# Kernel tuning notes

Measured on AMD Instinct MI355X. Metric: run time of the kernel, lower is better.

The kernel has to match this reference:

```python
import jax, jax.numpy as jnp
import numpy as np

N = 100000  # number of nodes
E = 3200000  # number of edges (avg degree 32)


def spmm(rows, cols, vals, Y):
    # sparse A (COO) @ dense Y : gather rows of Y at cols, scale, scatter-add to rows
    return jax.ops.segment_sum(vals[:, None] * Y[cols], rows, num_segments=N)


def setup_inputs() -> dict:
    key = jax.random.key(0)
    kx, kr, kc, kv, k0, k1 = jax.random.split(key, 6)
    X = jax.random.normal(kx, (N, 512), dtype=jnp.float32)
    edge_rows = jax.random.randint(kr, (E,), 0, N, dtype=jnp.int32)
    edge_cols = jax.random.randint(kc, (E,), 0, N, dtype=jnp.int32)
    edge_vals = jax.random.uniform(kv, (E,), dtype=jnp.float32)
    W0 = jax.random.normal(k0, (512, 256), dtype=jnp.float32) * 0.05
    W1 = jax.random.normal(k1, (256, 64), dtype=jnp.float32) * 0.05
    return {"X": X, "edge_rows": edge_rows, "edge_cols": edge_cols,
            "edge_vals": edge_vals, "W0": W0, "W1": W1}


def reference(X, edge_rows, edge_cols, edge_vals, W0, W1):
    # layer 1: A_hat @ (X W0), relu
    H1 = jax.nn.relu(spmm(edge_rows, edge_cols, edge_vals, X @ W0))  # [N, H]
    # layer 2: A_hat @ (H1 W1), softmax over classes
    Z = spmm(edge_rows, edge_cols, edge_vals, H1 @ W1)  # [N, F]
    return jax.nn.softmax(Z, axis=-1)
```

## Files before the change

### kernel.cpp

```cpp
#include <hip/hip_runtime.h>
#include <hip/hip_bf16.h>
#include <hip/hip_fp16.h>
#include <cstdint>

#define N_NODES 100000
#define N_EDGES 3200000
#define F_IN    512
#define F_HID   256
#define F_OUT   64
#define CAP     96

typedef _Float16 half8_t __attribute__((ext_vector_type(8)));
typedef _Float16 half4_t __attribute__((ext_vector_type(4)));
typedef float    float4_t __attribute__((ext_vector_type(4)));


__global__ __launch_bounds__(256) void zero_cursors_kernel(int* __restrict__ cursor, int n) {
    int i = blockIdx.x * 256 + threadIdx.x;
    if (i < n) cursor[i] = 0;
}

__global__ __launch_bounds__(256) void ell_scatter_kernel(
    const int* __restrict__ rows, const int* __restrict__ cols,
    const float* __restrict__ vals, int* __restrict__ cursor,
    int* __restrict__ ell_col, float* __restrict__ ell_val, int e_count) {
    int e = blockIdx.x * 256 + threadIdx.x;
    if (e >= e_count) return;
    int r = rows[e];
    int p = atomicAdd(&cursor[r], 1);
    if (p < CAP) {
        ell_col[(size_t)r * CAP + p] = cols[e];
        ell_val[(size_t)r * CAP + p] = vals[e];
    }
}


__global__ __launch_bounds__(256) void convert_w_kernel(
    const float* __restrict__ W0, const float* __restrict__ W1,
    _Float16* __restrict__ W0T, _Float16* __restrict__ W1T) {
    int i = blockIdx.x * 256 + threadIdx.x;
    if (i < F_HID * F_IN) {
        int n = i >> 9, k = i & 511;
        W0T[i] = (_Float16)W0[k * F_HID + n];
    }
    int j = i - F_HID * F_IN;
    if (j >= 0 && j < F_OUT * F_HID) {
        int n = j >> 8, k = j & 255;
        W1T[j] = (_Float16)W1[k * F_OUT + n];
    }
}


__global__ __launch_bounds__(256) void gemm1_mfma_kernel(
    const float* __restrict__ X, const _Float16* __restrict__ W0T,
    _Float16* __restrict__ H0) {
    const int wave = threadIdx.x >> 6;
    const int lane = threadIdx.x & 63;
    const int l15  = lane & 15;
    const int quad = lane >> 4;
    const int m0   = blockIdx.x * 64;
    const int n0   = wave * 64;

    float4_t acc[4][4] = {};

    int row[4];
    #pragma unroll
    for (int mt = 0; mt < 4; mt++) {
        int r = m0 + mt * 16 + l15;
        row[mt] = r < N_NODES ? r : N_NODES - 1;
    }

    for (int k0 = 0; k0 < F_IN; k0 += 32) {
        const int kk = k0 + quad * 8;
        half8_t b[4];
        #pragma unroll
        for (int nt = 0; nt < 4; nt++)
            b[nt] = *(const half8_t*)(W0T + (size_t)(n0 + nt * 16 + l15) * F_IN + kk);

        half8_t a[4];
        #pragma unroll
        for (int mt = 0; mt < 4; mt++) {
            const float* p = X + (size_t)row[mt] * F_IN + kk;
            float4_t lo = *(const float4_t*)p;
            float4_t hi = *(const float4_t*)(p + 4);
            half8_t f;
            f[0] = (_Float16)lo[0]; f[1] = (_Float16)lo[1];
            f[2] = (_Float16)lo[2]; f[3] = (_Float16)lo[3];
            f[4] = (_Float16)hi[0]; f[5] = (_Float16)hi[1];
            f[6] = (_Float16)hi[2]; f[7] = (_Float16)hi[3];
            a[mt] = f;
        }

        #pragma unroll
        for (int mt = 0; mt < 4; mt++)
            #pragma unroll
            for (int nt = 0; nt < 4; nt++)
                acc[mt][nt] = __builtin_amdgcn_mfma_f32_16x16x32_f16(
                    a[mt], b[nt], acc[mt][nt], 0, 0, 0);
    }

    #pragma unroll
    for (int mt = 0; mt < 4; mt++)
        #pragma unroll
        for (int reg = 0; reg < 4; reg++) {
            int m = m0 + mt * 16 + quad * 4 + reg;
            if (m < N_NODES) {
                #pragma unroll
                for (int nt = 0; nt < 4; nt++)
                    H0[(size_t)m * F_HID + n0 + nt * 16 + l15] =
                        (_Float16)acc[mt][nt][reg];
            }
        }
}


__global__ __launch_bounds__(256) void gemm2_mfma_kernel(
    const _Float16* __restrict__ H1, const _Float16* __restrict__ W1T,
    _Float16* __restrict__ H2) {
    const int wave = threadIdx.x >> 6;
    const int lane = threadIdx.x & 63;
    const int l15  = lane & 15;
    const int quad = lane >> 4;
    const int m0   = blockIdx.x * 64 + wave * 16;

    int r = m0 + l15;
    if (r >= N_NODES) r = N_NODES - 1;

    float4_t acc[4] = {};

    for (int k0 = 0; k0 < F_HID; k0 += 32) {
        const int kk = k0 + quad * 8;
        half8_t a = *(const half8_t*)(H1 + (size_t)r * F_HID + kk);
        #pragma unroll
        for (int nt = 0; nt < 4; nt++) {
            half8_t b = *(const half8_t*)(W1T + (size_t)(nt * 16 + l15) * F_HID + kk);
            acc[nt] = __builtin_amdgcn_mfma_f32_16x16x32_f16(a, b, acc[nt], 0, 0, 0);
        }
    }

    #pragma unroll
    for (int reg = 0; reg < 4; reg++) {
        int m = m0 + quad * 4 + reg;
        if (m < N_NODES) {
            #pragma unroll
            for (int nt = 0; nt < 4; nt++)
                H2[(size_t)m * F_OUT + nt * 16 + l15] = (_Float16)acc[nt][reg];
        }
    }
}


__global__ __launch_bounds__(256) void spmm_relu_kernel(
    const _Float16* __restrict__ H0, const int* __restrict__ ell_col,
    const float* __restrict__ ell_val, const int* __restrict__ cursor,
    _Float16* __restrict__ H1) {
    const int r = blockIdx.x * 4 + (threadIdx.x >> 6);
    const int t = threadIdx.x & 63;
    int n = cursor[r]; if (n > CAP) n = CAP;
    const int*   cols = ell_col + (size_t)r * CAP;
    const float* vals = ell_val + (size_t)r * CAP;
    const half4_t* H0v = (const half4_t*)H0;

    float4_t acc = {};
    int j = 0;
    for (; j + 4 <= n; j += 4) {
        int4   c = *(const int4*)(cols + j);
        float4 v = *(const float4*)(vals + j);
        half4_t g0 = H0v[(size_t)c.x * 64 + t];
        half4_t g1 = H0v[(size_t)c.y * 64 + t];
        half4_t g2 = H0v[(size_t)c.z * 64 + t];
        half4_t g3 = H0v[(size_t)c.w * 64 + t];
        #pragma unroll
        for (int i = 0; i < 4; i++) {
            acc[i] = fmaf(v.x, (float)g0[i], acc[i]);
            acc[i] = fmaf(v.y, (float)g1[i], acc[i]);
            acc[i] = fmaf(v.z, (float)g2[i], acc[i]);
            acc[i] = fmaf(v.w, (float)g3[i], acc[i]);
        }
    }
    for (; j < n; j++) {
        half4_t g = H0v[(size_t)cols[j] * 64 + t];
        float vv = vals[j];
        #pragma unroll
        for (int i = 0; i < 4; i++) acc[i] = fmaf(vv, (float)g[i], acc[i]);
    }
    half4_t o;
    #pragma unroll
    for (int i = 0; i < 4; i++) o[i] = (_Float16)fmaxf(acc[i], 0.f);
    ((half4_t*)H1)[(size_t)r * 64 + t] = o;
}


__global__ __launch_bounds__(256) void spmm_softmax_kernel(
    const _Float16* __restrict__ H2, const int* __restrict__ ell_col,
    const float* __restrict__ ell_val, const int* __restrict__ cursor,
    float* __restrict__ out) {
    const int lane = threadIdx.x & 63;
    const int r = blockIdx.x * 4 + (threadIdx.x >> 6);
    int n = cursor[r]; if (n > CAP) n = CAP;
    const int*   cols = ell_col + (size_t)r * CAP;
    const float* vals = ell_val + (size_t)r * CAP;
    float acc = 0.f;
    int j = 0;
    for (; j + 4 <= n; j += 4) {
        int4   c = *(const int4*)(cols + j);
        float4 v = *(const float4*)(vals + j);
        acc = fmaf(v.x, (float)H2[(size_t)c.x * F_OUT + lane], acc);
        acc = fmaf(v.y, (float)H2[(size_t)c.y * F_OUT + lane], acc);
        acc = fmaf(v.z, (float)H2[(size_t)c.z * F_OUT + lane], acc);
        acc = fmaf(v.w, (float)H2[(size_t)c.w * F_OUT + lane], acc);
    }
    for (; j < n; j++)
        acc = fmaf(vals[j], (float)H2[(size_t)cols[j] * F_OUT + lane], acc);

    float m = acc;
    #pragma unroll
    for (int o = 32; o >= 1; o >>= 1) m = fmaxf(m, __shfl_xor(m, o, 64));
    float e = expf(acc - m);
    float s = e;
    #pragma unroll
    for (int o = 32; o >= 1; o >>= 1) s += __shfl_xor(s, o, 64);
    out[(size_t)r * F_OUT + lane] = e / s;
}


extern "C" void kernel_launch(void* const* d_in, const int* in_sizes, int n_in,
                              void* d_out, int out_size, void* d_ws, size_t ws_size,
                              hipStream_t stream) {
    const float* X     = (const float*)d_in[0];
    const int*   erows = (const int*)  d_in[1];
    const int*   ecols = (const int*)  d_in[2];
    const float* evals = (const float*)d_in[3];
    const float* W0    = (const float*)d_in[4];
    const float* W1    = (const float*)d_in[5];
    float* out = (float*)d_out;

    char* p = (char*)d_ws;
    _Float16* H0  = (_Float16*)p; p += (size_t)N_NODES * F_HID * 2;
    _Float16* H1  = (_Float16*)p; p += (size_t)N_NODES * F_HID * 2;
    _Float16* H2  = (_Float16*)p; p += (size_t)N_NODES * F_OUT * 2;
    _Float16* W0T = (_Float16*)p; p += (size_t)F_HID * F_IN * 2;
    _Float16* W1T = (_Float16*)p; p += (size_t)F_OUT * F_HID * 2;
    int*   cursor  = (int*)p;     p += (size_t)N_NODES * 4;
    int*   ell_col = (int*)p;     p += (size_t)N_NODES * CAP * 4;
    float* ell_val = (float*)p;

    zero_cursors_kernel<<<(N_NODES + 255) / 256, 256, 0, stream>>>(cursor, N_NODES);
    ell_scatter_kernel<<<(N_EDGES + 255) / 256, 256, 0, stream>>>(
        erows, ecols, evals, cursor, ell_col, ell_val, N_EDGES);
    convert_w_kernel<<<(F_HID * F_IN + F_OUT * F_HID + 255) / 256, 256, 0, stream>>>(
        W0, W1, W0T, W1T);

    gemm1_mfma_kernel<<<(N_NODES + 63) / 64, 256, 0, stream>>>(X, W0T, H0);

    spmm_relu_kernel<<<N_NODES / 4, 256, 0, stream>>>(H0, ell_col, ell_val, cursor, H1);

    gemm2_mfma_kernel<<<(N_NODES + 63) / 64, 256, 0, stream>>>(H1, W1T, H2);

    spmm_softmax_kernel<<<N_NODES / 4, 256, 0, stream>>>(H2, ell_col, ell_val, cursor, out);
}
```

Baseline: 989.0 us.

## Fuse scatter with GEMM1, SpMM1 with GEMM2, and interleave ELL col/val

```diff
diff --git a/kernel.cpp b/kernel.cpp
--- a/kernel.cpp
+++ b/kernel.cpp
@@ -10,35 +10,21 @@
 #define F_OUT   64
 #define CAP     96
 
+#define G_SCATTER 12500
+#define G_GEMM1   3125
+#define LDS_STRIDE 272
+
 typedef _Float16 half8_t __attribute__((ext_vector_type(8)));
 typedef _Float16 half4_t __attribute__((ext_vector_type(4)));
 typedef float    float4_t __attribute__((ext_vector_type(4)));
 
 
-__global__ __launch_bounds__(256) void zero_cursors_kernel(int* __restrict__ cursor, int n) {
+__global__ __launch_bounds__(256) void prep_kernel(
+    const float* __restrict__ W0, const float* __restrict__ W1,
+    _Float16* __restrict__ W0T, _Float16* __restrict__ W1T,
+    int* __restrict__ cursor) {
     int i = blockIdx.x * 256 + threadIdx.x;
-    if (i < n) cursor[i] = 0;
-}
-
-__global__ __launch_bounds__(256) void ell_scatter_kernel(
-    const int* __restrict__ rows, const int* __restrict__ cols,
-    const float* __restrict__ vals, int* __restrict__ cursor,
-    int* __restrict__ ell_col, float* __restrict__ ell_val, int e_count) {
-    int e = blockIdx.x * 256 + threadIdx.x;
-    if (e >= e_count) return;
-    int r = rows[e];
-    int p = atomicAdd(&cursor[r], 1);
-    if (p < CAP) {
-        ell_col[(size_t)r * CAP + p] = cols[e];
-        ell_val[(size_t)r * CAP + p] = vals[e];
-    }
-}
-
-
-__global__ __launch_bounds__(256) void convert_w_kernel(
-    const float* __restrict__ W0, const float* __restrict__ W1,
-    _Float16* __restrict__ W0T, _Float16* __restrict__ W1T) {
-    int i = blockIdx.x * 256 + threadIdx.x;
+    if (i < N_NODES) cursor[i] = 0;
     if (i < F_HID * F_IN) {
         int n = i >> 9, k = i & 511;
         W0T[i] = (_Float16)W0[k * F_HID + n];
@@ -51,24 +37,31 @@
 }
 
 
-__global__ __launch_bounds__(256) void gemm1_mfma_kernel(
+__global__ __launch_bounds__(256, 6) void mega_kernel(
+    const int* __restrict__ erows, const int* __restrict__ ecols,
+    const float* __restrict__ evals, int* __restrict__ cursor,
+    int2* __restrict__ ell,
     const float* __restrict__ X, const _Float16* __restrict__ W0T,
     _Float16* __restrict__ H0) {
+
+    if (blockIdx.x < G_SCATTER) {
+        int e = blockIdx.x * 256 + threadIdx.x;
+        int r = erows[e];
+        int p = atomicAdd(&cursor[r], 1);
+        if (p < CAP)
+            ell[(size_t)r * CAP + p] = make_int2(ecols[e], __float_as_int(evals[e]));
+        return;
+    }
+
+    const int blk  = blockIdx.x - G_SCATTER;
     const int wave = threadIdx.x >> 6;
     const int lane = threadIdx.x & 63;
     const int l15  = lane & 15;
     const int quad = lane >> 4;
-    const int m0   = blockIdx.x * 64;
+    const int m0   = blk * 32;
     const int n0   = wave * 64;
 
-    float4_t acc[4][4] = {};
-
-    int row[4];
-    #pragma unroll
-    for (int mt = 0; mt < 4; mt++) {
-        int r = m0 + mt * 16 + l15;
-        row[mt] = r < N_NODES ? r : N_NODES - 1;
-    }
+    float4_t acc[2][4] = {};
 
     for (int k0 = 0; k0 < F_IN; k0 += 32) {
         const int kk = k0 + quad * 8;
@@ -77,10 +70,10 @@
         for (int nt = 0; nt < 4; nt++)
             b[nt] = *(const half8_t*)(W0T + (size_t)(n0 + nt * 16 + l15) * F_IN + kk);
 
-        half8_t a[4];
-        #pragma unroll
-        for (int mt = 0; mt < 4; mt++) {
-            const float* p = X + (size_t)row[mt] * F_IN + kk;
+        half8_t a[2];
+        #pragma unroll
+        for (int mt = 0; mt < 2; mt++) {
+            const float* p = X + (size_t)(m0 + mt * 16 + l15) * F_IN + kk;
             float4_t lo = *(const float4_t*)p;
             float4_t hi = *(const float4_t*)(p + 4);
             half8_t f;
@@ -92,7 +85,7 @@
         }
 
         #pragma unroll
-        for (int mt = 0; mt < 4; mt++)
+        for (int mt = 0; mt < 2; mt++)
             #pragma unroll
             for (int nt = 0; nt < 4; nt++)
                 acc[mt][nt] = __builtin_amdgcn_mfma_f32_16x16x32_f16(
@@ -100,118 +93,108 @@
     }
 
     #pragma unroll
-    for (int mt = 0; mt < 4; mt++)
+    for (int mt = 0; mt < 2; mt++)
         #pragma unroll
         for (int reg = 0; reg < 4; reg++) {
             int m = m0 + mt * 16 + quad * 4 + reg;
-            if (m < N_NODES) {
-                #pragma unroll
-                for (int nt = 0; nt < 4; nt++)
-                    H0[(size_t)m * F_HID + n0 + nt * 16 + l15] =
-                        (_Float16)acc[mt][nt][reg];
+            #pragma unroll
+            for (int nt = 0; nt < 4; nt++)
+                H0[(size_t)m * F_HID + n0 + nt * 16 + l15] =
+                    (_Float16)acc[mt][nt][reg];
+        }
+}
+
+
+__global__ __launch_bounds__(256) void spmm_relu_gemm2_kernel(
+    const _Float16* __restrict__ H0, const int2* __restrict__ ell,
+    const int* __restrict__ cursor, const _Float16* __restrict__ W1T,
+    _Float16* __restrict__ H2) {
+    __shared__ _Float16 hrow[16][LDS_STRIDE];
+
+    const int wave = threadIdx.x >> 6;
+    const int t    = threadIdx.x & 63;
+    const int base = blockIdx.x * 16;
+    const half4_t* H0v = (const half4_t*)H0;
+
+    for (int rr = 0; rr < 4; rr++) {
+        const int local = wave * 4 + rr;
+        const int r = base + local;
+        int n = cursor[r]; if (n > CAP) n = CAP;
+        const int2* cv = ell + (size_t)r * CAP;
+
+        float4_t acc = {};
+        int j = 0;
+        for (; j + 4 <= n; j += 4) {
+            int4 e0 = *(const int4*)(cv + j);
+            int4 e1 = *(const int4*)(cv + j + 2);
+            half4_t g0 = H0v[(size_t)e0.x * 64 + t];
+            half4_t g1 = H0v[(size_t)e0.z * 64 + t];
+            half4_t g2 = H0v[(size_t)e1.x * 64 + t];
+            half4_t g3 = H0v[(size_t)e1.z * 64 + t];
+            float v0 = __int_as_float(e0.y), v1 = __int_as_float(e0.w);
+            float v2 = __int_as_float(e1.y), v3 = __int_as_float(e1.w);
+            #pragma unroll
+            for (int i = 0; i < 4; i++) {
+                acc[i] = fmaf(v0, (float)g0[i], acc[i]);
+                acc[i] = fmaf(v1, (float)g1[i], acc[i]);
+                acc[i] = fmaf(v2, (float)g2[i], acc[i]);
+                acc[i] = fmaf(v3, (float)g3[i], acc[i]);
             }
         }
-}
-
-
-__global__ __launch_bounds__(256) void gemm2_mfma_kernel(
-    const _Float16* __restrict__ H1, const _Float16* __restrict__ W1T,
-    _Float16* __restrict__ H2) {
-    const int wave = threadIdx.x >> 6;
-    const int lane = threadIdx.x & 63;
-    const int l15  = lane & 15;
-    const int quad = lane >> 4;
-    const int m0   = blockIdx.x * 64 + wave * 16;
-
-    int r = m0 + l15;
-    if (r >= N_NODES) r = N_NODES - 1;
-
-    float4_t acc[4] = {};
-
+        for (; j < n; j++) {
+            int2 e = cv[j];
+            half4_t g = H0v[(size_t)e.x * 64 + t];
+            float vv = __int_as_float(e.y);
+            #pragma unroll
+            for (int i = 0; i < 4; i++) acc[i] = fmaf(vv, (float)g[i], acc[i]);
+        }
+        half4_t o;
+        #pragma unroll
+        for (int i = 0; i < 4; i++) o[i] = (_Float16)fmaxf(acc[i], 0.f);
+        *(half4_t*)(&hrow[local][t * 4]) = o;
+    }
+    __syncthreads();
+
+    const int l15  = t & 15;
+    const int quad = t >> 4;
+    float4_t acc2 = {};
+    #pragma unroll
     for (int k0 = 0; k0 < F_HID; k0 += 32) {
         const int kk = k0 + quad * 8;
-        half8_t a = *(const half8_t*)(H1 + (size_t)r * F_HID + kk);
-        #pragma unroll
-        for (int nt = 0; nt < 4; nt++) {
-            half8_t b = *(const half8_t*)(W1T + (size_t)(nt * 16 + l15) * F_HID + kk);
-            acc[nt] = __builtin_amdgcn_mfma_f32_16x16x32_f16(a, b, acc[nt], 0, 0, 0);
-        }
-    }
-
+        half8_t a = *(const half8_t*)(&hrow[l15][kk]);
+        half8_t b = *(const half8_t*)(W1T + (size_t)(wave * 16 + l15) * F_HID + kk);
+        acc2 = __builtin_amdgcn_mfma_f32_16x16x32_f16(a, b, acc2, 0, 0, 0);
+    }
     #pragma unroll
     for (int reg = 0; reg < 4; reg++) {
-        int m = m0 + quad * 4 + reg;
-        if (m < N_NODES) {
-            #pragma unroll
-            for (int nt = 0; nt < 4; nt++)
-                H2[(size_t)m * F_OUT + nt * 16 + l15] = (_Float16)acc[nt][reg];
-        }
-    }
-}
-
-
-__global__ __launch_bounds__(256) void spmm_relu_kernel(
-    const _Float16* __restrict__ H0, const int* __restrict__ ell_col,
-    const float* __restrict__ ell_val, const int* __restrict__ cursor,
-    _Float16* __restrict__ H1) {
-    const int r = blockIdx.x * 4 + (threadIdx.x >> 6);
-    const int t = threadIdx.x & 63;
-    int n = cursor[r]; if (n > CAP) n = CAP;
-    const int*   cols = ell_col + (size_t)r * CAP;
-    const float* vals = ell_val + (size_t)r * CAP;
-    const half4_t* H0v = (const half4_t*)H0;
-
-    float4_t acc = {};
-    int j = 0;
-    for (; j + 4 <= n; j += 4) {
-        int4   c = *(const int4*)(cols + j);
-        float4 v = *(const float4*)(vals + j);
-        half4_t g0 = H0v[(size_t)c.x * 64 + t];
-        half4_t g1 = H0v[(size_t)c.y * 64 + t];
-        half4_t g2 = H0v[(size_t)c.z * 64 + t];
-        half4_t g3 = H0v[(size_t)c.w * 64 + t];
-        #pragma unroll
-        for (int i = 0; i < 4; i++) {
-            acc[i] = fmaf(v.x, (float)g0[i], acc[i]);
-            acc[i] = fmaf(v.y, (float)g1[i], acc[i]);
-            acc[i] = fmaf(v.z, (float)g2[i], acc[i]);
-            acc[i] = fmaf(v.w, (float)g3[i], acc[i]);
-        }
-    }
-    for (; j < n; j++) {
-        half4_t g = H0v[(size_t)cols[j] * 64 + t];
-        float vv = vals[j];
-        #pragma unroll
-        for (int i = 0; i < 4; i++) acc[i] = fmaf(vv, (float)g[i], acc[i]);
-    }
-    half4_t o;
-    #pragma unroll
-    for (int i = 0; i < 4; i++) o[i] = (_Float16)fmaxf(acc[i], 0.f);
-    ((half4_t*)H1)[(size_t)r * 64 + t] = o;
+        int m = base + quad * 4 + reg;
+        H2[(size_t)m * F_OUT + wave * 16 + l15] = (_Float16)acc2[reg];
+    }
 }
 
 
 __global__ __launch_bounds__(256) void spmm_softmax_kernel(
-    const _Float16* __restrict__ H2, const int* __restrict__ ell_col,
-    const float* __restrict__ ell_val, const int* __restrict__ cursor,
-    float* __restrict__ out) {
+    const _Float16* __restrict__ H2, const int2* __restrict__ ell,
+    const int* __restrict__ cursor, float* __restrict__ out) {
     const int lane = threadIdx.x & 63;
     const int r = blockIdx.x * 4 + (threadIdx.x >> 6);
     int n = cursor[r]; if (n > CAP) n = CAP;
-    const int*   cols = ell_col + (size_t)r * CAP;
-    const float* vals = ell_val + (size_t)r * CAP;
+    const int2* cv = ell + (size_t)r * CAP;
+
     float acc = 0.f;
     int j = 0;
     for (; j + 4 <= n; j += 4) {
-        int4   c = *(const int4*)(cols + j);
-        float4 v = *(const float4*)(vals + j);
-        acc = fmaf(v.x, (float)H2[(size_t)c.x * F_OUT + lane], acc);
-        acc = fmaf(v.y, (float)H2[(size_t)c.y * F_OUT + lane], acc);
-        acc = fmaf(v.z, (float)H2[(size_t)c.z * F_OUT + lane], acc);
-        acc = fmaf(v.w, (float)H2[(size_t)c.w * F_OUT + lane], acc);
-    }
-    for (; j < n; j++)
-        acc = fmaf(vals[j], (float)H2[(size_t)cols[j] * F_OUT + lane], acc);
+        int4 e0 = *(const int4*)(cv + j);
+        int4 e1 = *(const int4*)(cv + j + 2);
+        acc = fmaf(__int_as_float(e0.y), (float)H2[(size_t)e0.x * F_OUT + lane], acc);
+        acc = fmaf(__int_as_float(e0.w), (float)H2[(size_t)e0.z * F_OUT + lane], acc);
+        acc = fmaf(__int_as_float(e1.y), (float)H2[(size_t)e1.x * F_OUT + lane], acc);
+        acc = fmaf(__int_as_float(e1.w), (float)H2[(size_t)e1.z * F_OUT + lane], acc);
+    }
+    for (; j < n; j++) {
+        int2 e = cv[j];
+        acc = fmaf(__int_as_float(e.y), (float)H2[(size_t)e.x * F_OUT + lane], acc);
+    }
 
     float m = acc;
     #pragma unroll
@@ -237,25 +220,18 @@
 
     char* p = (char*)d_ws;
     _Float16* H0  = (_Float16*)p; p += (size_t)N_NODES * F_HID * 2;
-    _Float16* H1  = (_Float16*)p; p += (size_t)N_NODES * F_HID * 2;
     _Float16* H2  = (_Float16*)p; p += (size_t)N_NODES * F_OUT * 2;
     _Float16* W0T = (_Float16*)p; p += (size_t)F_HID * F_IN * 2;
     _Float16* W1T = (_Float16*)p; p += (size_t)F_OUT * F_HID * 2;
-    int*   cursor  = (int*)p;     p += (size_t)N_NODES * 4;
-    int*   ell_col = (int*)p;     p += (size_t)N_NODES * CAP * 4;
-    float* ell_val = (float*)p;
-
-    zero_cursors_kernel<<<(N_NODES + 255) / 256, 256, 0, stream>>>(cursor, N_NODES);
-    ell_scatter_kernel<<<(N_EDGES + 255) / 256, 256, 0, stream>>>(
-        erows, ecols, evals, cursor, ell_col, ell_val, N_EDGES);
-    convert_w_kernel<<<(F_HID * F_IN + F_OUT * F_HID + 255) / 256, 256, 0, stream>>>(
-        W0, W1, W0T, W1T);
-
-    gemm1_mfma_kernel<<<(N_NODES + 63) / 64, 256, 0, stream>>>(X, W0T, H0);
-
-    spmm_relu_kernel<<<N_NODES / 4, 256, 0, stream>>>(H0, ell_col, ell_val, cursor, H1);
-
-    gemm2_mfma_kernel<<<(N_NODES + 63) / 64, 256, 0, stream>>>(H1, W1T, H2);
-
-    spmm_softmax_kernel<<<N_NODES / 4, 256, 0, stream>>>(H2, ell_col, ell_val, cursor, out);
-}
+    int*  cursor  = (int*)p;      p += (size_t)N_NODES * 4;
+    int2* ell     = (int2*)p;
+
+    prep_kernel<<<576, 256, 0, stream>>>(W0, W1, W0T, W1T, cursor);
+
+    mega_kernel<<<G_SCATTER + G_GEMM1, 256, 0, stream>>>(
+        erows, ecols, evals, cursor, ell, X, W0T, H0);
+
+    spmm_relu_gemm2_kernel<<<N_NODES / 16, 256, 0, stream>>>(H0, ell, cursor, W1T, H2);
+
+    spmm_softmax_kernel<<<N_NODES / 4, 256, 0, stream>>>(H2, ell, cursor, out);
+}
```

After: 1.007 ms. About the same (+1.9%).
